# Kernel optimization log

Hardware: AMD Instinct MI355X
Metric: run time of the kernel (lower is better)

## Reference

```python
import math
import jax, jax.numpy as jnp
import numpy as np

B, C, H, W = 64, 32, 224, 224
MINDEV = np.float32(1.0 / math.sqrt(H * W))


def setup_inputs() -> dict:
    key = jax.random.key(0)
    x = jax.random.normal(key, (B, C, H, W), dtype=jnp.float32)
    return {"x": x}


def reference(x):
    # Per-(batch, channel) mean and unbiased std over the HxW slice,
    # matching torch.std's default ddof=1.
    m = jnp.mean(x, axis=(2, 3), keepdims=True)
    s = jnp.std(x, axis=(2, 3), keepdims=True, ddof=1)
    # Cap std away from zero: dev = max(std, 1/sqrt(H*W))
    s = jnp.maximum(s, jnp.asarray(MINDEV, x.dtype))
    return (x - m) / s
```

## Files before the change

kernel.cpp:

```cpp
#include <hip/hip_runtime.h>
#include <math.h>


namespace {
constexpr int   kHW        = 224 * 224;
constexpr int   kHW4       = kHW / 4;
constexpr int   kThreads   = 1024;
constexpr int   kWaves     = kThreads / 64;
constexpr int   kPerBlock  = 8;
constexpr int   kBlocks    = (64 * 32) / kPerBlock;
constexpr int   kAFull     = 6;
constexpr int   kAExtraOff = kAFull * kThreads;
constexpr int   kAExtraCnt = 256;
constexpr int   kBOff      = 6400;
constexpr int   kBFull     = 6;
constexpr float kMinDev    = 1.0f / 224.0f;

typedef float vfloat4 __attribute__((ext_vector_type(4)));
}

__global__ __launch_bounds__(kThreads, 4)
void whiten_pipe3(const float* __restrict__ x, float* __restrict__ y) {
    __shared__ float2 wred[2][kWaves];

    const int  tid  = threadIdx.x;
    const int  wid  = tid >> 6;
    const int  lane = tid & 63;
    const bool ea   = (tid < kAExtraCnt);
    const size_t base = (size_t)blockIdx.x * kPerBlock * kHW4;
    const vfloat4* __restrict__ xs = reinterpret_cast<const vfloat4*>(x) + base;
    vfloat4* __restrict__ ys       = reinterpret_cast<vfloat4*>(y) + base;

    vfloat4 b0[7], b1[7], b2[7];

    auto loadA = [&](vfloat4 (&B)[7], int s) {
        const vfloat4* __restrict__ p = xs + (size_t)s * kHW4;
#pragma unroll
        for (int i = 0; i < kAFull; ++i) B[i] = p[i * kThreads + tid];
        if (ea) B[6] = p[kAExtraOff + tid];
    };
    auto loadB = [&](vfloat4 (&B)[7], int s) {
        const vfloat4* __restrict__ p = xs + (size_t)s * kHW4 + kBOff;
#pragma unroll
        for (int i = 0; i < kBFull; ++i) B[i] = p[i * kThreads + tid];
    };
    auto acc1 = [&](const vfloat4& v, float& sum, float& ssq) {
        sum += v.x + v.y + v.z + v.w;
        ssq = fmaf(v.x, v.x, ssq);
        ssq = fmaf(v.y, v.y, ssq);
        ssq = fmaf(v.z, v.z, ssq);
        ssq = fmaf(v.w, v.w, ssq);
    };
    auto accA = [&](vfloat4 (&B)[7], float& sum, float& ssq) {
#pragma unroll
        for (int i = 0; i < kAFull; ++i) acc1(B[i], sum, ssq);
        if (ea) acc1(B[6], sum, ssq);
    };
    auto accB = [&](vfloat4 (&B)[7], float& sum, float& ssq) {
#pragma unroll
        for (int i = 0; i < kBFull; ++i) acc1(B[i], sum, ssq);
    };
    auto norm1 = [&](const vfloat4& v, float mean, float rcp) {
        vfloat4 o;
        o.x = (v.x - mean) * rcp;
        o.y = (v.y - mean) * rcp;
        o.z = (v.z - mean) * rcp;
        o.w = (v.w - mean) * rcp;
        return o;
    };

    auto slice = [&](vfloat4 (&P)[7], vfloat4 (&Q)[7], vfloat4 (&R)[7],
                     int s, bool pre, float sum, float ssq) -> float2 {
        if (pre) loadA(R, s + 1);
        accB(Q, sum, ssq);
#pragma unroll
        for (int off = 32; off >= 1; off >>= 1) {
            sum += __shfl_down(sum, off, 64);
            ssq += __shfl_down(ssq, off, 64);
        }
        if (lane == 0) wred[s & 1][wid] = make_float2(sum, ssq);
        asm volatile("s_waitcnt lgkmcnt(0)\n\ts_barrier" ::: "memory");
        float S = 0.f, SS = 0.f;
#pragma unroll
        for (int i = 0; i < kWaves; ++i) {
            S += wred[s & 1][i].x;
            SS += wred[s & 1][i].y;
        }
        const float mean = S * (1.0f / kHW);
        float var = (SS - S * mean) * (1.0f / (kHW - 1));
        var = fmaxf(var, 0.f);
        const float rcp = 1.0f / fmaxf(sqrtf(var), kMinDev);

        vfloat4* __restrict__ pa = ys + (size_t)s * kHW4;
#pragma unroll
        for (int i = 0; i < kAFull; ++i)
            pa[i * kThreads + tid] = norm1(P[i], mean, rcp);
        if (ea) pa[kAExtraOff + tid] = norm1(P[6], mean, rcp);
        vfloat4* __restrict__ pb = pa + kBOff;
#pragma unroll
        for (int i = 0; i < kBFull; ++i)
            pb[i * kThreads + tid] = norm1(Q[i], mean, rcp);

        float ns = 0.f, nq = 0.f;
        if (pre) {
            loadB(P, s + 1);
            accA(R, ns, nq);
        }
        return make_float2(ns, nq);
    };

    loadA(b0, 0);
    loadB(b1, 0);
    float sum = 0.f, ssq = 0.f;
    accA(b0, sum, ssq);

    float2 c;
    c = slice(b0, b1, b2, 0, true, sum, ssq);
    c = slice(b2, b0, b1, 1, true, c.x, c.y);
    c = slice(b1, b2, b0, 2, true, c.x, c.y);
    c = slice(b0, b1, b2, 3, true, c.x, c.y);
    c = slice(b2, b0, b1, 4, true, c.x, c.y);
    c = slice(b1, b2, b0, 5, true, c.x, c.y);
    c = slice(b0, b1, b2, 6, true, c.x, c.y);
    (void)slice(b2, b0, b1, 7, false, c.x, c.y);
}

extern "C" void kernel_launch(void* const* d_in, const int* in_sizes, int n_in,
                              void* d_out, int out_size, void* d_ws, size_t ws_size,
                              hipStream_t stream) {
    (void)in_sizes; (void)n_in; (void)d_ws; (void)ws_size; (void)out_size;
    const float* x = reinterpret_cast<const float*>(d_in[0]);
    float* y = reinterpret_cast<float*>(d_out);
    whiten_pipe3<<<kBlocks, kThreads, 0, stream>>>(x, y);
}
```

Baseline: 166.4 us.

## Replace triple-buffer slice pipeline with two-buffer overlap that refills after stores

```diff
diff --git a/kernel.cpp b/kernel.cpp
--- a/kernel.cpp
+++ b/kernel.cpp
@@ -3,46 +3,47 @@
 
 
 namespace {
-constexpr int   kHW        = 224 * 224;
-constexpr int   kHW4       = kHW / 4;
-constexpr int   kThreads   = 1024;
-constexpr int   kWaves     = kThreads / 64;
-constexpr int   kPerBlock  = 8;
-constexpr int   kBlocks    = (64 * 32) / kPerBlock;
-constexpr int   kAFull     = 6;
-constexpr int   kAExtraOff = kAFull * kThreads;
-constexpr int   kAExtraCnt = 256;
-constexpr int   kBOff      = 6400;
-constexpr int   kBFull     = 6;
-constexpr float kMinDev    = 1.0f / 224.0f;
+constexpr int   kHW       = 224 * 224;
+constexpr int   kHW4      = kHW / 4;
+constexpr int   kThreads  = 1024;
+constexpr int   kWaves    = kThreads / 64;
+constexpr int   kPerBlock = 8;
+constexpr int   kBlocks   = (64 * 32) / kPerBlock;
+constexpr int   kPreRows  = 5;
+constexpr int   kMainRows = 7;
+constexpr int   kQOff     = 12 * kThreads;
+constexpr int   kQCnt     = kHW4 - kQOff;
+constexpr float kMinDev   = 1.0f / 224.0f;
 
 typedef float vfloat4 __attribute__((ext_vector_type(4)));
 }
 
 __global__ __launch_bounds__(kThreads, 4)
-void whiten_pipe3(const float* __restrict__ x, float* __restrict__ y) {
+void whiten_overlap(const float* __restrict__ x, float* __restrict__ y) {
     __shared__ float2 wred[2][kWaves];
 
     const int  tid  = threadIdx.x;
     const int  wid  = tid >> 6;
     const int  lane = tid & 63;
-    const bool ea   = (tid < kAExtraCnt);
+    const bool q    = (tid < kQCnt);
     const size_t base = (size_t)blockIdx.x * kPerBlock * kHW4;
     const vfloat4* __restrict__ xs = reinterpret_cast<const vfloat4*>(x) + base;
     vfloat4* __restrict__ ys       = reinterpret_cast<vfloat4*>(y) + base;
 
-    vfloat4 b0[7], b1[7], b2[7];
+    vfloat4 mn[kMainRows + 1];
+    vfloat4 pre[kPreRows];
 
-    auto loadA = [&](vfloat4 (&B)[7], int s) {
+    auto issueMain = [&](int s) {
         const vfloat4* __restrict__ p = xs + (size_t)s * kHW4;
 #pragma unroll
-        for (int i = 0; i < kAFull; ++i) B[i] = p[i * kThreads + tid];
-        if (ea) B[6] = p[kAExtraOff + tid];
+        for (int i = 0; i < kMainRows; ++i)
+            mn[i] = p[(kPreRows + i) * kThreads + tid];
+        if (q) mn[kMainRows] = p[kQOff + tid];
     };
-    auto loadB = [&](vfloat4 (&B)[7], int s) {
-        const vfloat4* __restrict__ p = xs + (size_t)s * kHW4 + kBOff;
+    auto issuePre = [&](int s) {
+        const vfloat4* __restrict__ p = xs + (size_t)s * kHW4;
 #pragma unroll
-        for (int i = 0; i < kBFull; ++i) B[i] = p[i * kThreads + tid];
+        for (int i = 0; i < kPreRows; ++i) pre[i] = p[i * kThreads + tid];
     };
     auto acc1 = [&](const vfloat4& v, float& sum, float& ssq) {
         sum += v.x + v.y + v.z + v.w;
@@ -50,15 +51,6 @@
         ssq = fmaf(v.y, v.y, ssq);
         ssq = fmaf(v.z, v.z, ssq);
         ssq = fmaf(v.w, v.w, ssq);
-    };
-    auto accA = [&](vfloat4 (&B)[7], float& sum, float& ssq) {
-#pragma unroll
-        for (int i = 0; i < kAFull; ++i) acc1(B[i], sum, ssq);
-        if (ea) acc1(B[6], sum, ssq);
-    };
-    auto accB = [&](vfloat4 (&B)[7], float& sum, float& ssq) {
-#pragma unroll
-        for (int i = 0; i < kBFull; ++i) acc1(B[i], sum, ssq);
     };
     auto norm1 = [&](const vfloat4& v, float mean, float rcp) {
         vfloat4 o;
@@ -69,10 +61,14 @@
         return o;
     };
 
-    auto slice = [&](vfloat4 (&P)[7], vfloat4 (&Q)[7], vfloat4 (&R)[7],
-                     int s, bool pre, float sum, float ssq) -> float2 {
-        if (pre) loadA(R, s + 1);
-        accB(Q, sum, ssq);
+    auto step = [&](int s, bool prefetchNext) {
+        float sum = 0.f, ssq = 0.f;
+#pragma unroll
+        for (int i = 0; i < kMainRows; ++i) acc1(mn[i], sum, ssq);
+        if (q) acc1(mn[kMainRows], sum, ssq);
+#pragma unroll
+        for (int i = 0; i < kPreRows; ++i) acc1(pre[i], sum, ssq);
+
 #pragma unroll
         for (int off = 32; off >= 1; off >>= 1) {
             sum += __shfl_down(sum, off, 64);
@@ -80,6 +76,7 @@
         }
         if (lane == 0) wred[s & 1][wid] = make_float2(sum, ssq);
         asm volatile("s_waitcnt lgkmcnt(0)\n\ts_barrier" ::: "memory");
+
         float S = 0.f, SS = 0.f;
 #pragma unroll
         for (int i = 0; i < kWaves; ++i) {
@@ -91,38 +88,23 @@
         var = fmaxf(var, 0.f);
         const float rcp = 1.0f / fmaxf(sqrtf(var), kMinDev);
 
-        vfloat4* __restrict__ pa = ys + (size_t)s * kHW4;
+        vfloat4* __restrict__ p = ys + (size_t)s * kHW4;
 #pragma unroll
-        for (int i = 0; i < kAFull; ++i)
-            pa[i * kThreads + tid] = norm1(P[i], mean, rcp);
-        if (ea) pa[kAExtraOff + tid] = norm1(P[6], mean, rcp);
-        vfloat4* __restrict__ pb = pa + kBOff;
+        for (int i = 0; i < kMainRows; ++i)
+            p[(kPreRows + i) * kThreads + tid] = norm1(mn[i], mean, rcp);
+        if (q) p[kQOff + tid] = norm1(mn[kMainRows], mean, rcp);
+        if (prefetchNext) issueMain(s + 1);
 #pragma unroll
-        for (int i = 0; i < kBFull; ++i)
-            pb[i * kThreads + tid] = norm1(Q[i], mean, rcp);
-
-        float ns = 0.f, nq = 0.f;
-        if (pre) {
-            loadB(P, s + 1);
-            accA(R, ns, nq);
-        }
-        return make_float2(ns, nq);
+        for (int i = 0; i < kPreRows; ++i)
+            p[i * kThreads + tid] = norm1(pre[i], mean, rcp);
+        if (prefetchNext) issuePre(s + 1);
     };
 
-    loadA(b0, 0);
-    loadB(b1, 0);
-    float sum = 0.f, ssq = 0.f;
-    accA(b0, sum, ssq);
-
-    float2 c;
-    c = slice(b0, b1, b2, 0, true, sum, ssq);
-    c = slice(b2, b0, b1, 1, true, c.x, c.y);
-    c = slice(b1, b2, b0, 2, true, c.x, c.y);
-    c = slice(b0, b1, b2, 3, true, c.x, c.y);
-    c = slice(b2, b0, b1, 4, true, c.x, c.y);
-    c = slice(b1, b2, b0, 5, true, c.x, c.y);
-    c = slice(b0, b1, b2, 6, true, c.x, c.y);
-    (void)slice(b2, b0, b1, 7, false, c.x, c.y);
+    issueMain(0);
+    issuePre(0);
+#pragma unroll 1
+    for (int s = 0; s < kPerBlock - 1; ++s) step(s, true);
+    step(kPerBlock - 1, false);
 }
 
 extern "C" void kernel_launch(void* const* d_in, const int* in_sizes, int n_in,
@@ -131,5 +113,5 @@
     (void)in_sizes; (void)n_in; (void)d_ws; (void)ws_size; (void)out_size;
     const float* x = reinterpret_cast<const float*>(d_in[0]);
     float* y = reinterpret_cast<float*>(d_out);
-    whiten_pipe3<<<kBlocks, kThreads, 0, stream>>>(x, y);
+    whiten_overlap<<<kBlocks, kThreads, 0, stream>>>(x, y);
 }
```

New measurement: 166.1 us. About the same (-0.2%).
